# Optimization experiments

Measured on AMD Instinct MI355X. Metric: run time of the kernel, lower is better.

The kernel has to match this reference:

```python
import jax, jax.numpy as jnp
import numpy as np

NUM_GRAPHS = 128


def _gcn_conv(x, W, b, src, dst, norm, n_nodes):
    # PyG GCNConv: linear transform, then symmetric-normalized scatter-add aggregation
    h = x @ W                                  # [N, out]
    msg = norm[:, None] * h[src]               # [E+N, out] gathered messages
    out = jax.ops.segment_sum(msg, dst, num_segments=n_nodes)
    return out + b


def setup_inputs() -> dict:
    key = jax.random.key(0)
    ks = jax.random.split(key, 12)
    N, E, H, GE, C = 100000, 1000000, 64, 64, 5
    x = jax.random.normal(ks[0], (N, 2), dtype=jnp.float32)
    edge_index = jax.random.randint(ks[1], (2, E), 0, N, dtype=jnp.int32)
    batch = jnp.sort(jax.random.randint(ks[2], (N,), 0, NUM_GRAPHS, dtype=jnp.int32))
    graph_embedding = jax.random.normal(ks[3], (NUM_GRAPHS, GE), dtype=jnp.float32)
    s = lambda k, shape, fan: jax.random.normal(k, shape, dtype=jnp.float32) * (1.0 / np.sqrt(fan))
    W1 = s(ks[4], (2, H), 2); b1 = jnp.zeros((H,), jnp.float32)
    W2 = s(ks[5], (H, H), H); b2 = jnp.zeros((H,), jnp.float32)
    W3 = s(ks[6], (H, H), H); b3 = jnp.zeros((H,), jnp.float32)
    Wl = s(ks[7], (H + GE, C), H + GE); bl = jnp.zeros((C,), jnp.float32)
    return {"x": x, "edge_index": edge_index, "batch": batch,
            "graph_embedding": graph_embedding,
            "W1": W1, "b1": b1, "W2": W2, "b2": b2, "W3": W3, "b3": b3,
            "Wl": Wl, "bl": bl}


def reference(x, edge_index, batch, graph_embedding, W1, b1, W2, b2, W3, b3, Wl, bl):
    N = x.shape[0]
    loops = jnp.arange(N, dtype=edge_index.dtype)
    src = jnp.concatenate([edge_index[0], loops])   # add self-loops
    dst = jnp.concatenate([edge_index[1], loops])
    deg = jax.ops.segment_sum(jnp.ones_like(dst, dtype=x.dtype), dst, num_segments=N)
    dinv = jnp.where(deg > 0, jax.lax.rsqrt(deg), 0.0)
    norm = dinv[src] * dinv[dst]                    # [E+N]

    h = jax.nn.relu(_gcn_conv(x, W1, b1, src, dst, norm, N))
    h = jax.nn.relu(_gcn_conv(h, W2, b2, src, dst, norm, N))
    h = _gcn_conv(h, W3, b3, src, dst, norm, N)

    # global mean pool over graphs
    sums = jax.ops.segment_sum(h, batch, num_segments=NUM_GRAPHS)
    cnts = jax.ops.segment_sum(jnp.ones((N,), x.dtype), batch, num_segments=NUM_GRAPHS)
    pooled = sums / jnp.maximum(cnts, 1.0)[:, None]

    z = jnp.concatenate([pooled, graph_embedding], axis=1) @ Wl + bl
    return jax.nn.log_softmax(z, axis=1)
```

## Files before the change

kernel.cpp:

```cpp
#include <hip/hip_runtime.h>
#include <hip/hip_bf16.h>
#include <math.h>

#define NG 128
#define CHUNKB 4096
#define NBIN 512
#define EWIN 256
#define STAGE_CAP 6144

typedef __attribute__((ext_vector_type(8))) short short8;
typedef __attribute__((ext_vector_type(4))) float float4v;

__global__ void k_bin_hist(const int* __restrict__ dst, int* __restrict__ hist,
                           int e, int nb, float* __restrict__ sums,
                           const float* __restrict__ W2, const float* __restrict__ W3,
                           __hip_bfloat16* __restrict__ Wf2, __hip_bfloat16* __restrict__ Wf3) {
    __shared__ int h[NBIN];
    int blk = blockIdx.x;
    if (blk >= nb) {
        int ex = blk - nb;
        if (ex == 0) {
            for (int i = threadIdx.x; i < NG * 64; i += 256) sums[i] = 0.0f;
        } else {
            const float* W = (ex == 2) ? W3 : W2;
            __hip_bfloat16* Wf = (ex == 2) ? Wf3 : Wf2;
            for (int t = threadIdx.x; t < 512; t += 256) {
                int c = t >> 6, l = t & 63;
                int jt = c >> 1, half = c & 1, nn = l & 15, q = l >> 4;
                #pragma unroll
                for (int j = 0; j < 8; j++) {
                    int k = half * 32 + q * 8 + j;
                    Wf[t * 8 + j] = __float2bfloat16(W[k * 64 + jt * 16 + nn]);
                }
            }
        }
        return;
    }
    for (int i = threadIdx.x; i < NBIN; i += 256) h[i] = 0;
    __syncthreads();
    int base = blk * CHUNKB;
    int lim = e - base; if (lim > CHUNKB) lim = CHUNKB;
    for (int k = threadIdx.x; k < lim; k += 256)
        atomicAdd(&h[dst[base + k] >> 8], 1);
    __syncthreads();
    for (int b = threadIdx.x; b < NBIN; b += 256) hist[b * nb + blk] = h[b];
}

__global__ void __launch_bounds__(512) genscan1(int* __restrict__ a, int* __restrict__ bsums, int n) {
    __shared__ int s[512];
    int tid = threadIdx.x;
    int i = blockIdx.x * 512 + tid;
    int v = (i < n) ? a[i] : 0;
    s[tid] = v;
    __syncthreads();
    for (int d = 1; d < 512; d <<= 1) {
        int t = (tid >= d) ? s[tid - d] : 0;
        __syncthreads();
        s[tid] += t;
        __syncthreads();
    }
    if (i < n) a[i] = s[tid] - v;
    if (tid == 511) bsums[blockIdx.x] = s[511];
}

__global__ void __launch_bounds__(512) genscan2(int* __restrict__ bsums, int nb) {
    __shared__ int s[512];
    int tid = threadIdx.x;
    int v = (tid < nb) ? bsums[tid] : 0;
    s[tid] = v;
    __syncthreads();
    for (int d = 1; d < 512; d <<= 1) {
        int t = (tid >= d) ? s[tid - d] : 0;
        __syncthreads();
        s[tid] += t;
        __syncthreads();
    }
    if (tid < nb) bsums[tid] = s[tid] - v;
}

__global__ void k_bin_scatter(const int* __restrict__ srcs, const int* __restrict__ dsts,
                              const int* __restrict__ offsets, const int* __restrict__ bsums,
                              int2* __restrict__ outbuf, int e, int nb) {
    __shared__ int hcnt[NBIN];
    __shared__ int lstart[NBIN];
    __shared__ int ss[256];
    __shared__ int2 stage[CHUNKB];
    int tid = threadIdx.x, blk = blockIdx.x, base = blk * CHUNKB;
    int lim = e - base; if (lim > CHUNKB) lim = CHUNKB;
    for (int i = tid; i < NBIN; i += 256) hcnt[i] = 0;
    __syncthreads();
    for (int k = tid; k < lim; k += 256)
        atomicAdd(&hcnt[dsts[base + k] >> 8], 1);
    __syncthreads();
    int c0 = hcnt[2 * tid], c1 = hcnt[2 * tid + 1];
    int sum = c0 + c1;
    ss[tid] = sum;
    __syncthreads();
    for (int d = 1; d < 256; d <<= 1) {
        int t = (tid >= d) ? ss[tid - d] : 0;
        __syncthreads();
        ss[tid] += t;
        __syncthreads();
    }
    int excl = ss[tid] - sum;
    lstart[2 * tid] = excl;
    lstart[2 * tid + 1] = excl + c0;
    __syncthreads();
    hcnt[2 * tid] = excl;
    hcnt[2 * tid + 1] = excl + c0;
    __syncthreads();
    for (int k = tid; k < lim; k += 256) {
        int2 ed = make_int2(srcs[base + k], dsts[base + k]);
        int p = atomicAdd(&hcnt[ed.y >> 8], 1);
        stage[p] = ed;
    }
    __syncthreads();
    for (int i = tid; i < NBIN; i += 256) {
        int gi = i * nb + blk;
        lstart[i] = offsets[gi] + bsums[gi >> 9] - lstart[i];
    }
    __syncthreads();
    for (int p = tid; p < lim; p += 256) {
        int2 ed = stage[p];
        outbuf[lstart[ed.y >> 8] + p] = ed;
    }
}

__global__ void k_csrAB(const int2* __restrict__ ebuck, const int* __restrict__ offsets,
                        const int* __restrict__ bsums, const float* __restrict__ x,
                        int* __restrict__ row_ptr, float* __restrict__ dinv,
                        float2* __restrict__ xs, int* __restrict__ csr,
                        int n, int nb, int e_total) {
    __shared__ int lcnt[256];
    __shared__ int ssc[256];
    __shared__ int rstart[256];
    __shared__ int2 stage[STAGE_CAP];
    int b = blockIdx.x, tid = threadIdx.x, n0 = b << 8;
    lcnt[tid] = 0;
    __syncthreads();
    int i0 = b * nb, i1 = (b + 1) * nb;
    int e0 = offsets[i0] + bsums[i0 >> 9];
    int e1 = offsets[i1] + bsums[i1 >> 9];
    int cnt = e1 - e0;
    bool fast = (cnt <= STAGE_CAP);
    if (fast) {
        for (int i = e0 + tid; i < e1; i += 256) {
            int2 ed = ebuck[i];
            stage[i - e0] = ed;
            atomicAdd(&lcnt[ed.y - n0], 1);
        }
    } else {
        for (int i = e0 + tid; i < e1; i += 256)
            atomicAdd(&lcnt[ebuck[i].y - n0], 1);
    }
    __syncthreads();
    int v = lcnt[tid];
    ssc[tid] = v;
    __syncthreads();
    for (int d = 1; d < 256; d <<= 1) {
        int t = (tid >= d) ? ssc[tid - d] : 0;
        __syncthreads();
        ssc[tid] += t;
        __syncthreads();
    }
    int rs = e0 + ssc[tid] - v;
    rstart[tid] = rs;
    int node = n0 + tid;
    if (node < n) {
        row_ptr[node] = rs;
        float dv = rsqrtf((float)v + 1.0f);
        dinv[node] = dv;
        const float2* x2 = (const float2*)x;
        float2 xi = x2[node];
        xs[node] = make_float2(xi.x * dv, xi.y * dv);
        if (node == n - 1) row_ptr[n] = e_total;
    }
    lcnt[tid] = 0;
    __syncthreads();
    if (fast) {
        for (int i = tid; i < cnt; i += 256) {
            int2 ed = stage[i];
            int li = ed.y - n0;
            int r = atomicAdd(&lcnt[li], 1);
            csr[rstart[li] + r] = ed.x;
        }
    } else {
        for (int i = e0 + tid; i < e1; i += 256) {
            int2 ed = ebuck[i];
            int li = ed.y - n0;
            int r = atomicAdd(&lcnt[li], 1);
            csr[rstart[li] + r] = ed.x;
        }
    }
}

__global__ void k_layer1(const int* __restrict__ row_ptr, const int* __restrict__ edges,
                         const float2* __restrict__ xs, const float* __restrict__ dinv,
                         const float* __restrict__ W1, const float* __restrict__ b1,
                         __hip_bfloat16* __restrict__ h, int n) {
    __shared__ float w1s[128];
    __shared__ float b1s[64];
    if (threadIdx.x < 128) w1s[threadIdx.x] = W1[threadIdx.x];
    if (threadIdx.x < 64) b1s[threadIdx.x] = b1[threadIdx.x];
    __syncthreads();
    int i = blockIdx.x * blockDim.x + threadIdx.x;
    if (i >= n) return;
    float dd = dinv[i];
    float2 xi = xs[i];
    float a0 = xi.x, a1 = xi.y;
    int lo = row_ptr[i], hi = row_ptr[i + 1];
    int k = lo;
    for (; k + 4 <= hi; k += 4) {
        int s0 = edges[k], s1 = edges[k + 1], s2 = edges[k + 2], s3 = edges[k + 3];
        float2 v0 = xs[s0], v1 = xs[s1], v2 = xs[s2], v3 = xs[s3];
        a0 += v0.x + v1.x + v2.x + v3.x;
        a1 += v0.y + v1.y + v2.y + v3.y;
    }
    for (; k < hi; k++) {
        float2 v = xs[edges[k]];
        a0 += v.x;
        a1 += v.y;
    }
    a0 *= dd; a1 *= dd;
    short8* hv = reinterpret_cast<short8*>(h + (size_t)i * 64);
    #pragma unroll
    for (int g = 0; g < 8; g++) {
        short8 pack;
        #pragma unroll
        for (int j = 0; j < 8; j++) {
            int col = g * 8 + j;
            float v = fmaxf(a0 * w1s[col] + a1 * w1s[64 + col] + b1s[col], 0.0f);
            v *= dd;
            __hip_bfloat16 bv = __float2bfloat16(v);
            pack[j] = *reinterpret_cast<short*>(&bv);
        }
        hv[g] = pack;
    }
}

template <bool FAST>
static __device__ __forceinline__ void agg_node(int lo, int hi, int half, int col,
        const int* __restrict__ gE, const int* EW, int wave_lo,
        const uint* __restrict__ hinu, float& ax, float& ay) {
    for (int k = lo; k < hi; k += 16) {
        int ss[8];
        #pragma unroll
        for (int j = 0; j < 8; j++) {
            int idx = k + 2 * j + half;
            int cidx = idx < hi ? idx : lo;
            ss[j] = FAST ? EW[cidx - wave_lo] : gE[cidx];
        }
        uint vv[8];
        #pragma unroll
        for (int j = 0; j < 8; j++) vv[j] = hinu[(size_t)ss[j] * 32 + col];
        #pragma unroll
        for (int j = 0; j < 8; j++) {
            int idx = k + 2 * j + half;
            uint u = idx < hi ? vv[j] : 0u;
            ax += __int_as_float(u << 16);
            ay += __int_as_float(u & 0xffff0000u);
        }
    }
}

template <int RELU, int POOL>
__global__ void __launch_bounds__(64, 8) k_aggLin(const int* __restrict__ row_ptr,
                                                  const int* __restrict__ edges,
                                                  const __hip_bfloat16* __restrict__ hin,
                                                  const float* __restrict__ dinv,
                                                  const __hip_bfloat16* __restrict__ Wf,
                                                  const float* __restrict__ b,
                                                  __hip_bfloat16* __restrict__ hout,
                                                  const int* __restrict__ batch,
                                                  float* __restrict__ sums, int n) {
    __shared__ __attribute__((aligned(16))) __hip_bfloat16 T[16 * 72];
    __shared__ int EW[EWIN];
    int lane = threadIdx.x;
    int nb0 = blockIdx.x * 16;
    if (nb0 >= n) return;
    int half = lane >> 5, col = lane & 31;
    const uint* hinu = reinterpret_cast<const uint*>(hin);

    int bidx = nb0 + (lane < 16 ? lane : 16);
    if (bidx > n) bidx = n;
    int rp = row_ptr[bidx];
    int wave_lo = __shfl(rp, 0);
    int wave_hi = __shfl(rp, 16);
    int cnt = wave_hi - wave_lo;
    bool fast = (cnt <= EWIN);
    if (fast)
        for (int i = lane; i < cnt; i += 64) EW[i] = edges[wave_lo + i];

    for (int nn = 0; nn < 16; nn++) {
        int node = nb0 + nn;
        float ax = 0.0f, ay = 0.0f;
        if (node < n) {
            if (half == 0) {
                uint hv = hinu[(size_t)node * 32 + col];
                ax = __int_as_float(hv << 16);
                ay = __int_as_float(hv & 0xffff0000u);
            }
            int lo = __shfl(rp, nn), hi = __shfl(rp, nn + 1);
            if (fast) agg_node<true >(lo, hi, half, col, edges, EW, wave_lo, hinu, ax, ay);
            else      agg_node<false>(lo, hi, half, col, edges, EW, wave_lo, hinu, ax, ay);
        }
        ax += __shfl_xor(ax, 32);
        ay += __shfl_xor(ay, 32);
        if (half == 0) {
            float dv = dinv[node < n ? node : 0];
            ax *= dv; ay *= dv;
            __hip_bfloat16 bx = __float2bfloat16(ax);
            __hip_bfloat16 by = __float2bfloat16(ay);
            uint pack = (uint)(*reinterpret_cast<unsigned short*>(&bx)) |
                        ((uint)(*reinterpret_cast<unsigned short*>(&by)) << 16);
            *reinterpret_cast<uint*>(&T[nn * 72 + 2 * col]) = pack;
        }
    }

    int m = lane & 15, q = lane >> 4;
    short8 a0 = *reinterpret_cast<const short8*>(&T[m * 72 + q * 8]);
    short8 a1 = *reinterpret_cast<const short8*>(&T[m * 72 + 32 + q * 8]);
    int lastn = nb0 + 15 < n ? nb0 + 15 : n - 1;
    bool onegraph = POOL && (nb0 + 15 < n) && (batch[nb0] == batch[lastn]);
    int gA = POOL ? batch[nb0] : 0;
    float dvs[4];
    if (!POOL) {
        #pragma unroll
        for (int r = 0; r < 4; r++) {
            int node = nb0 + q * 4 + r;
            dvs[r] = node < n ? dinv[node] : 0.0f;
        }
    }
    #pragma unroll
    for (int jt = 0; jt < 4; jt++) {
        short8 bf0 = *reinterpret_cast<const short8*>(Wf + ((size_t)(jt * 2 + 0) * 64 + lane) * 8);
        short8 bf1 = *reinterpret_cast<const short8*>(Wf + ((size_t)(jt * 2 + 1) * 64 + lane) * 8);
        float4v d = {0.0f, 0.0f, 0.0f, 0.0f};
        d = __builtin_amdgcn_mfma_f32_16x16x32_bf16(a0, bf0, d, 0, 0, 0);
        d = __builtin_amdgcn_mfma_f32_16x16x32_bf16(a1, bf1, d, 0, 0, 0);
        float bias = b[jt * 16 + m];
        if (POOL) {
            if (onegraph) {
                float s = (d[0] + bias) + (d[1] + bias) + (d[2] + bias) + (d[3] + bias);
                s += __shfl_xor(s, 16);
                s += __shfl_xor(s, 32);
                if (q == 0) atomicAdd(&sums[gA * 64 + jt * 16 + m], s);
            } else {
                #pragma unroll
                for (int r = 0; r < 4; r++) {
                    int node = nb0 + q * 4 + r;
                    if (node < n)
                        atomicAdd(&sums[batch[node] * 64 + jt * 16 + m], d[r] + bias);
                }
            }
        } else {
            #pragma unroll
            for (int r = 0; r < 4; r++) {
                int node = nb0 + q * 4 + r;
                if (node < n) {
                    float v = d[r] + bias;
                    if (RELU) v = fmaxf(v, 0.0f);
                    v *= dvs[r];
                    hout[(size_t)node * 64 + jt * 16 + m] = __float2bfloat16(v);
                }
            }
        }
    }
}

__device__ inline int lower_bound_i(const int* __restrict__ a, int n, int key) {
    int lo = 0, hi = n;
    while (lo < hi) {
        int mid = (lo + hi) >> 1;
        if (a[mid] < key) lo = mid + 1; else hi = mid;
    }
    return lo;
}

__global__ void k_head(const float* __restrict__ sums, const int* __restrict__ batch,
                       const float* __restrict__ ge, const float* __restrict__ Wl,
                       const float* __restrict__ bl, float* __restrict__ out,
                       int n, int ng) {
    int g = blockIdx.x * blockDim.x + threadIdx.x;
    if (g < ng) {
        int lo = lower_bound_i(batch, n, g);
        int hi = lower_bound_i(batch, n, g + 1);
        float c = fmaxf((float)(hi - lo), 1.0f);
        float z[5];
        for (int cl = 0; cl < 5; cl++) z[cl] = bl[cl];
        for (int k = 0; k < 64; k++) {
            float p = sums[g * 64 + k] / c;
            for (int cl = 0; cl < 5; cl++) z[cl] += p * Wl[k * 5 + cl];
        }
        for (int k = 0; k < 64; k++) {
            float p = ge[g * 64 + k];
            for (int cl = 0; cl < 5; cl++) z[cl] += p * Wl[(64 + k) * 5 + cl];
        }
        float m = z[0];
        for (int cl = 1; cl < 5; cl++) m = fmaxf(m, z[cl]);
        float s = 0.0f;
        for (int cl = 0; cl < 5; cl++) s += expf(z[cl] - m);
        float lse = m + logf(s);
        for (int cl = 0; cl < 5; cl++) out[g * 5 + cl] = z[cl] - lse;
    }
}

#define ALIGN16(x) (((x) + 15) & ~(size_t)15)

extern "C" void kernel_launch(void* const* d_in, const int* in_sizes, int n_in,
                              void* d_out, int out_size, void* d_ws, size_t ws_size,
                              hipStream_t stream) {
    const float* x    = (const float*)d_in[0];
    const int*   ei   = (const int*)d_in[1];
    const int*   batch= (const int*)d_in[2];
    const float* ge   = (const float*)d_in[3];
    const float* W1   = (const float*)d_in[4];
    const float* b1   = (const float*)d_in[5];
    const float* W2   = (const float*)d_in[6];
    const float* b2   = (const float*)d_in[7];
    const float* W3   = (const float*)d_in[8];
    const float* b3   = (const float*)d_in[9];
    const float* Wl   = (const float*)d_in[10];
    const float* bl   = (const float*)d_in[11];
    float* out = (float*)d_out;

    const int N = in_sizes[0] / 2;
    const int E = in_sizes[1] / 2;
    const int* src = ei;
    const int* dst = ei + E;
    const int NBUK = (N + 255) >> 8;
    const int nbC  = (E + CHUNKB - 1) / CHUNKB;

    char* wsb = (char*)d_ws;
    float* dinv   = (float*)wsb;                wsb += ALIGN16((size_t)N * 4);
    float2* xs    = (float2*)wsb;               wsb += ALIGN16((size_t)N * 8);
    __hip_bfloat16* h16 = (__hip_bfloat16*)wsb;  wsb += ALIGN16((size_t)64 * N * 2);
    __hip_bfloat16* buf2= (__hip_bfloat16*)wsb;  wsb += ALIGN16((size_t)64 * N * 2);
    float* sums   = (float*)wsb;                wsb += ALIGN16((size_t)NG * 64 * 4);
    __hip_bfloat16* Wf2 = (__hip_bfloat16*)wsb; wsb += ALIGN16((size_t)4096 * 2);
    __hip_bfloat16* Wf3 = (__hip_bfloat16*)wsb; wsb += ALIGN16((size_t)4096 * 2);
    int2*  ebuck  = (int2*)wsb;                 wsb += ALIGN16((size_t)E * 8);
    int*   csr    = (int*)wsb;                  wsb += ALIGN16((size_t)E * 4);
    int*   row_ptr= (int*)wsb;                  wsb += ALIGN16((size_t)(N + 1) * 4);
    int*   hist   = (int*)wsb;                  wsb += ALIGN16((size_t)NBIN * nbC * 4);
    int*   bsums  = (int*)wsb;                  wsb += 512 * 4;

    const int BS = 256;
    int gN   = (N + BS - 1) / BS;
    int gF   = (N + 15) / 16;
    int nH   = NBIN * nbC;
    int gH   = (nH + 511) / 512;

    k_bin_hist<<<nbC + 3, BS, 0, stream>>>(dst, hist, E, nbC, sums, W2, W3, Wf2, Wf3);
    genscan1<<<gH, 512, 0, stream>>>(hist, bsums, nH);
    genscan2<<<1, 512, 0, stream>>>(bsums, gH);
    k_bin_scatter<<<nbC, BS, 0, stream>>>(src, dst, hist, bsums, ebuck, E, nbC);
    k_csrAB<<<NBUK, BS, 0, stream>>>(ebuck, hist, bsums, x, row_ptr, dinv, xs, csr,
                                     N, nbC, E);

    k_layer1<<<gN, BS, 0, stream>>>(row_ptr, csr, xs, dinv, W1, b1, h16, N);

    k_aggLin<1, 0><<<gF, 64, 0, stream>>>(row_ptr, csr, h16, dinv, Wf2, b2, buf2,
                                          nullptr, nullptr, N);

    k_aggLin<0, 1><<<gF, 64, 0, stream>>>(row_ptr, csr, buf2, dinv, Wf3, b3, nullptr,
                                          batch, sums, N);

    k_head<<<1, 128, 0, stream>>>(sums, batch, ge, Wl, bl, out, N, NG);
}
```

Baseline: 220.6 us.

## Aggregate eight nodes per wave with 16-byte vector gathers per lane

Restructures the neighbor aggregation so each wave handles 8 nodes at once, with 8 lanes per node each loading a 16-byte chunk (8 bf16 features) per neighbor row. This replaces the old scheme of one node per iteration with 32 lanes × 4 bytes split across two halves, and drops the cross-half shuffle reduction. The aim is wider memory transactions and more nodes in flight. The cost is divergence: each 8-node group loops to the maximum degree across the wave, so lanes with fewer neighbors do masked, wasted loads.

```diff
diff --git a/kernel.cpp b/kernel.cpp
--- a/kernel.cpp
+++ b/kernel.cpp
@@ -10,6 +10,7 @@
 
 typedef __attribute__((ext_vector_type(8))) short short8;
 typedef __attribute__((ext_vector_type(4))) float float4v;
+typedef __attribute__((ext_vector_type(4))) uint uint4v;
 
 __global__ void k_bin_hist(const int* __restrict__ dst, int* __restrict__ hist,
                            int e, int nb, float* __restrict__ sums,
@@ -238,28 +239,31 @@
     }
 }
 
+static __device__ __forceinline__ void acc8(float* a, uint4v v) {
+    #pragma unroll
+    for (int i = 0; i < 4; i++) {
+        uint u = v[i];
+        a[2 * i]     += __int_as_float(u << 16);
+        a[2 * i + 1] += __int_as_float(u & 0xffff0000u);
+    }
+}
+
 template <bool FAST>
-static __device__ __forceinline__ void agg_node(int lo, int hi, int half, int col,
+static __device__ __forceinline__ void agg_group(int lo, int cnt, int mc, int c,
         const int* __restrict__ gE, const int* EW, int wave_lo,
-        const uint* __restrict__ hinu, float& ax, float& ay) {
-    for (int k = lo; k < hi; k += 16) {
-        int ss[8];
-        #pragma unroll
-        for (int j = 0; j < 8; j++) {
-            int idx = k + 2 * j + half;
-            int cidx = idx < hi ? idx : lo;
-            ss[j] = FAST ? EW[cidx - wave_lo] : gE[cidx];
-        }
-        uint vv[8];
-        #pragma unroll
-        for (int j = 0; j < 8; j++) vv[j] = hinu[(size_t)ss[j] * 32 + col];
-        #pragma unroll
-        for (int j = 0; j < 8; j++) {
-            int idx = k + 2 * j + half;
-            uint u = idx < hi ? vv[j] : 0u;
-            ax += __int_as_float(u << 16);
-            ay += __int_as_float(u & 0xffff0000u);
-        }
+        const uint4v* __restrict__ hin4, float* acc) {
+    for (int j = 0; j < mc; j += 2) {
+        bool ok0 = j < cnt, ok1 = j + 1 < cnt;
+        int e0 = ok0 ? lo + j : wave_lo;
+        int e1 = ok1 ? lo + j + 1 : wave_lo;
+        int s0 = FAST ? EW[e0 - wave_lo] : gE[e0];
+        int s1 = FAST ? EW[e1 - wave_lo] : gE[e1];
+        uint4v v0 = hin4[(size_t)s0 * 8 + c];
+        uint4v v1 = hin4[(size_t)s1 * 8 + c];
+        if (!ok0) v0 = (uint4v){0u, 0u, 0u, 0u};
+        if (!ok1) v1 = (uint4v){0u, 0u, 0u, 0u};
+        acc8(acc, v0);
+        acc8(acc, v1);
     }
 }
 
@@ -278,43 +282,46 @@
     int lane = threadIdx.x;
     int nb0 = blockIdx.x * 16;
     if (nb0 >= n) return;
-    int half = lane >> 5, col = lane & 31;
-    const uint* hinu = reinterpret_cast<const uint*>(hin);
+    int g = lane >> 3;
+    int c = lane & 7;
+    const uint4v* hin4 = reinterpret_cast<const uint4v*>(hin);
 
     int bidx = nb0 + (lane < 16 ? lane : 16);
     if (bidx > n) bidx = n;
     int rp = row_ptr[bidx];
     int wave_lo = __shfl(rp, 0);
     int wave_hi = __shfl(rp, 16);
-    int cnt = wave_hi - wave_lo;
-    bool fast = (cnt <= EWIN);
+    int cnt_all = wave_hi - wave_lo;
+    bool fast = (cnt_all <= EWIN);
     if (fast)
-        for (int i = lane; i < cnt; i += 64) EW[i] = edges[wave_lo + i];
-
-    for (int nn = 0; nn < 16; nn++) {
+        for (int i = lane; i < cnt_all; i += 64) EW[i] = edges[wave_lo + i];
+
+    #pragma unroll
+    for (int h8 = 0; h8 < 2; h8++) {
+        int nn = h8 * 8 + g;
         int node = nb0 + nn;
-        float ax = 0.0f, ay = 0.0f;
-        if (node < n) {
-            if (half == 0) {
-                uint hv = hinu[(size_t)node * 32 + col];
-                ax = __int_as_float(hv << 16);
-                ay = __int_as_float(hv & 0xffff0000u);
-            }
-            int lo = __shfl(rp, nn), hi = __shfl(rp, nn + 1);
-            if (fast) agg_node<true >(lo, hi, half, col, edges, EW, wave_lo, hinu, ax, ay);
-            else      agg_node<false>(lo, hi, half, col, edges, EW, wave_lo, hinu, ax, ay);
-        }
-        ax += __shfl_xor(ax, 32);
-        ay += __shfl_xor(ay, 32);
-        if (half == 0) {
-            float dv = dinv[node < n ? node : 0];
-            ax *= dv; ay *= dv;
-            __hip_bfloat16 bx = __float2bfloat16(ax);
-            __hip_bfloat16 by = __float2bfloat16(ay);
-            uint pack = (uint)(*reinterpret_cast<unsigned short*>(&bx)) |
-                        ((uint)(*reinterpret_cast<unsigned short*>(&by)) << 16);
-            *reinterpret_cast<uint*>(&T[nn * 72 + 2 * col]) = pack;
-        }
+        float acc[8] = {0.f, 0.f, 0.f, 0.f, 0.f, 0.f, 0.f, 0.f};
+        int lo = __shfl(rp, nn);
+        int hi = __shfl(rp, nn + 1);
+        int cnt = (node < n) ? (hi - lo) : 0;
+        int mc = cnt;
+        mc = max(mc, __shfl_xor(mc, 8));
+        mc = max(mc, __shfl_xor(mc, 16));
+        mc = max(mc, __shfl_xor(mc, 32));
+        if (node < n)
+            acc8(acc, hin4[(size_t)node * 8 + c]);
+        if (fast) agg_group<true >(lo, cnt, mc, c, edges, EW, wave_lo, hin4, acc);
+        else      agg_group<false>(lo, cnt, mc, c, edges, EW, wave_lo, hin4, acc);
+        float dv = (node < n) ? dinv[node] : 0.0f;
+        uint4v pk;
+        #pragma unroll
+        for (int i = 0; i < 4; i++) {
+            __hip_bfloat16 bx = __float2bfloat16(acc[2 * i] * dv);
+            __hip_bfloat16 by = __float2bfloat16(acc[2 * i + 1] * dv);
+            pk[i] = (uint)(*reinterpret_cast<unsigned short*>(&bx)) |
+                    ((uint)(*reinterpret_cast<unsigned short*>(&by)) << 16);
+        }
+        *reinterpret_cast<uint4v*>(&T[nn * 72 + c * 8]) = pk;
     }
 
     int m = lane & 15, q = lane >> 4;
```

New measurement: 199.7 us. 1.1x faster.
